# Kernel tuning notes

Hardware: AMD Instinct MI355X
Metric: run time of the kernel (lower is better)

The kernel has to match this reference:

```python
import jax, jax.numpy as jnp
import numpy as np

B, T, H, OUT = 2048, 256, 512, 1


def setup_inputs() -> dict:
    key = jax.random.key(0)
    ks = jax.random.split(key, 11)
    s = 1.0 / np.sqrt(H)
    return {
        "x": jax.random.normal(ks[0], (B, T), dtype=jnp.float32),
        # weights stored as (in, out), i.e. torch Linear weight transposed
        "Wx0": jax.random.normal(ks[1], (1, H), dtype=jnp.float32) * s,
        "bx0": jax.random.normal(ks[2], (H,), dtype=jnp.float32) * s,
        "Wh0": jax.random.normal(ks[3], (H, H), dtype=jnp.float32) * s,
        "bh0": jax.random.normal(ks[4], (H,), dtype=jnp.float32) * s,
        "Wx1": jax.random.normal(ks[5], (H, H), dtype=jnp.float32) * s,
        "bx1": jax.random.normal(ks[6], (H,), dtype=jnp.float32) * s,
        "Wh1": jax.random.normal(ks[7], (H, H), dtype=jnp.float32) * s,
        "bh1": jax.random.normal(ks[8], (H,), dtype=jnp.float32) * s,
        "Wfc": jax.random.normal(ks[9], (H, OUT), dtype=jnp.float32) * s,
        "bfc": jax.random.normal(ks[10], (OUT,), dtype=jnp.float32) * s,
    }


def reference(x, Wx0, bx0, Wh0, bh0, Wx1, bx1, Wh1, bh1, Wfc, bfc):
    # Stacked 2-layer Elman RNN: h_l[t] = tanh(W_in_l @ in + b_in_l + W_h_l @ h_l[t-1] + b_h_l)
    batch = x.shape[0]
    hdim = Wh0.shape[0]
    h0 = jnp.zeros((batch, hdim), dtype=x.dtype)
    h1 = jnp.zeros((batch, hdim), dtype=x.dtype)

    def step(carry, xt):
        h0, h1 = carry
        # layer 0: scalar input per timestep -> outer product with Wx0 row
        h0 = jnp.tanh(xt[:, None] * Wx0[0] + bx0 + h0 @ Wh0 + bh0)
        # layer 1 consumes the NEW h0 (matches the in-place loop in torch)
        h1 = jnp.tanh(h0 @ Wx1 + bx1 + h1 @ Wh1 + bh1)
        return (h0, h1), None

    (h0, h1), _ = jax.lax.scan(step, (h0, h1), x.T)  # scan over time [T, B]
    return h1 @ Wfc + bfc  # [B, OUT]
```

## Files before the change

### kernel.cpp

```cpp
#include <hip/hip_runtime.h>
#include <hip/hip_bf16.h>


typedef _Float16 half8 __attribute__((ext_vector_type(8)));
typedef float f32x4 __attribute__((ext_vector_type(4)));

#define T_STEPS 256
#define H_DIM   512
#define BM      16

#define BARRIER() do { \
    asm volatile("s_waitcnt lgkmcnt(0)" ::: "memory"); \
    __builtin_amdgcn_s_barrier(); \
    asm volatile("" ::: "memory"); \
  } while (0)

__device__ __forceinline__ half8 gld16(const half8* p){
  half8 r;
  asm volatile("global_load_dwordx4 %0, %1, off" : "=v"(r) : "v"(p));
  return r;
}

__device__ __forceinline__ float tanh_fast(float z){
  float az = fabsf(z);
  float e  = __expf(-2.0f * az);
  float r  = (1.0f - e) * __builtin_amdgcn_rcpf(1.0f + e);
  return copysignf(r, z);
}

__global__ void prep_w_45028437131357(const float* __restrict__ W,
                                      half8* __restrict__ out){
  int tid  = blockIdx.x * 256 + threadIdx.x;
  int lane = tid & 63;
  int kc   = (tid >> 6) & 15;
  int nt   = tid >> 10;
  int col  = nt * 16 + (lane & 15);
  int k0   = kc * 32 + (lane >> 4) * 8;
  half8 v;
#pragma unroll
  for (int j = 0; j < 8; ++j) v[j] = (_Float16)W[(k0 + j) * H_DIM + col];
  out[tid] = v;
}


__global__ __launch_bounds__(512, 2)
void rnn_main_45028437131357(const float* __restrict__ x,
                             const float* __restrict__ Wx0,
                             const float* __restrict__ bx0,
                             const float* __restrict__ bh0,
                             const float* __restrict__ bx1,
                             const float* __restrict__ bh1,
                             const float* __restrict__ Wfc,
                             const float* __restrict__ bfc,
                             const half8* __restrict__ Wh0f,
                             const half8* __restrict__ Wx1f,
                             const half8* __restrict__ Wh1f,
                             float* __restrict__ out){
  __shared__ __align__(16) char  h0d[2][BM * 1024];
  __shared__ __align__(16) char  h1s[BM * 1024];
  __shared__ __align__(16) float xall[BM * 256];
  __shared__ char lds_pad[20 * 1024];

  const int tid  = threadIdx.x;
  const int lane = tid & 63;
  const int w    = tid >> 6;
  const int w4   = 4 * w;
  const int r0   = blockIdx.x * BM;
  const int koff = (blockIdx.x >> 3) & 15;

  if (out == nullptr) ((volatile char*)lds_pad)[0] = 1;

  for (int i = tid; i < BM * 256; i += 512){
    ((float*)h0d[0])[i] = 0.0f;
    ((float*)h1s)[i] = 0.0f;
    int r = i >> 8, c = i & 255;
    xall[r * 256 + (c ^ ((r & 7) << 2))] = x[(r0 + r) * T_STEPS + c];
  }

  const int cl      = lane & 15;
  const int kg      = lane >> 4;
  const int aBase   = cl * 1024 + kg * 16;
  const int aSwz    = (cl & 7) << 4;
  const int rowBase = kg * 4;

  float wx0c[4], b0c[4], b1c[4];
  int   colA[4];
#pragma unroll
  for (int i = 0; i < 4; ++i){
    int col = (w4 + i) * 16 + cl;
    colA[i] = col;
    wx0c[i] = Wx0[col];
    b0c[i]  = bx0[col] + bh0[col];
    b1c[i]  = bx1[col] + bh1[col];
  }

  half8 rb[4][4];

#define STAGE(G)                                                              \
  {                                                                           \
    int g48 = ((G) >= 48) ? (G) - 48 : (G);                                   \
    const half8* M = (g48 < 16) ? Wh0f : ((g48 < 32) ? Wh1f : Wx1f);          \
    int keff = ((g48 & 15) + koff) & 15;                                      \
    const half8* base = M + keff * 64 + lane;                                 \
    rb[(G) & 3][0] = gld16(base + (w4 + 0) * 1024);                           \
    rb[(G) & 3][1] = gld16(base + (w4 + 1) * 1024);                           \
    rb[(G) & 3][2] = gld16(base + (w4 + 2) * 1024);                           \
    rb[(G) & 3][3] = gld16(base + (w4 + 3) * 1024);                           \
  }

#define CONSUME(APTR, ACC, KC, G)                                             \
  {                                                                           \
    int keff = (((KC) + koff) & 15);                                          \
    half8 a = *(const half8*)((APTR) + ((aBase + keff * 64) ^ aSwz));         \
    asm volatile("s_waitcnt vmcnt(12)");                                      \
    __builtin_amdgcn_sched_barrier(0);                                        \
    ACC[0] = __builtin_amdgcn_mfma_f32_16x16x32_f16(a, rb[(G)&3][0], ACC[0], 0,0,0); \
    ACC[1] = __builtin_amdgcn_mfma_f32_16x16x32_f16(a, rb[(G)&3][1], ACC[1], 0,0,0); \
    ACC[2] = __builtin_amdgcn_mfma_f32_16x16x32_f16(a, rb[(G)&3][2], ACC[2], 0,0,0); \
    ACC[3] = __builtin_amdgcn_mfma_f32_16x16x32_f16(a, rb[(G)&3][3], ACC[3], 0,0,0); \
  }

  asm volatile("s_waitcnt vmcnt(0)" ::: "memory");
  STAGE(0); STAGE(1); STAGE(2);

  const f32x4 z4 = {0.f, 0.f, 0.f, 0.f};
  int s = 0;

  for (int t = 0; t < T_STEPS; ++t){
    BARRIER();

    const char* h0cur = h0d[s];
    char*       h0nxt = h0d[s ^ 1];

    f32x4 acc0[4] = {z4, z4, z4, z4};
    f32x4 acc1[4] = {z4, z4, z4, z4};

#pragma unroll
    for (int kc = 0; kc < 16; ++kc){
      STAGE(kc + 3);
      CONSUME(h0cur, acc0, kc, kc);
    }
#pragma unroll
    for (int kc = 0; kc < 16; ++kc){
      STAGE(kc + 19);
      CONSUME(h1s, acc1, kc, kc + 16);
    }

    {
      float xv[4];
#pragma unroll
      for (int rg = 0; rg < 4; ++rg){
        int row = rowBase + rg;
        xv[rg] = xall[row * 256 + (t ^ ((row & 7) << 2))];
      }
#pragma unroll
      for (int i = 0; i < 4; ++i)
#pragma unroll
        for (int rg = 0; rg < 4; ++rg){
          float z = acc0[i][rg] + b0c[i] + xv[rg] * wx0c[i];
          int row = rowBase + rg;
          *(_Float16*)(h0nxt + row * 1024 +
                       ((colA[i] * 2) ^ ((row & 7) << 4))) = (_Float16)tanh_fast(z);
        }
    }
    BARRIER();

#pragma unroll
    for (int kc = 0; kc < 16; ++kc){
      STAGE(kc + 35);
      CONSUME(h0nxt, acc1, kc, kc + 32);
    }

#pragma unroll
    for (int i = 0; i < 4; ++i)
#pragma unroll
      for (int rg = 0; rg < 4; ++rg){
        int row = rowBase + rg;
        *(_Float16*)(h1s + row * 1024 +
                     ((colA[i] * 2) ^ ((row & 7) << 4))) =
            (_Float16)tanh_fast(acc1[i][rg] + b1c[i]);
      }
    s ^= 1;
  }
#undef STAGE
#undef CONSUME

  asm volatile("s_waitcnt vmcnt(0)" ::: "memory");
  BARRIER();

  {
    int r  = tid >> 5;
    int g2 = tid & 31;
    float p = 0.0f;
#pragma unroll
    for (int k2 = 0; k2 < 16; ++k2){
      int c = g2 + 32 * k2;
      float hv = (float)*(const _Float16*)(h1s + r * 1024 +
                                           ((c * 2) ^ ((r & 7) << 4)));
      p += hv * Wfc[c];
    }
#pragma unroll
    for (int off = 16; off >= 1; off >>= 1) p += __shfl_xor(p, off);
    if (g2 == 0) out[r0 + r] = p + bfc[0];
  }
}

extern "C" void kernel_launch(void* const* d_in, const int* in_sizes, int n_in,
                              void* d_out, int out_size, void* d_ws, size_t ws_size,
                              hipStream_t stream) {
  const float* x   = (const float*)d_in[0];
  const float* Wx0 = (const float*)d_in[1];
  const float* bx0 = (const float*)d_in[2];
  const float* Wh0 = (const float*)d_in[3];
  const float* bh0 = (const float*)d_in[4];
  const float* Wx1 = (const float*)d_in[5];
  const float* bx1 = (const float*)d_in[6];
  const float* Wh1 = (const float*)d_in[7];
  const float* bh1 = (const float*)d_in[8];
  const float* Wfc = (const float*)d_in[9];
  const float* bfc = (const float*)d_in[10];

  _Float16* wsH = (_Float16*)d_ws;
  half8* Wh0f = (half8*)(wsH);
  half8* Wx1f = (half8*)(wsH + 262144);
  half8* Wh1f = (half8*)(wsH + 524288);

  prep_w_45028437131357<<<128, 256, 0, stream>>>(Wh0, Wh0f);
  prep_w_45028437131357<<<128, 256, 0, stream>>>(Wx1, Wx1f);
  prep_w_45028437131357<<<128, 256, 0, stream>>>(Wh1, Wh1f);

  rnn_main_45028437131357<<<128, 512, 0, stream>>>(
      x, Wx0, bx0, bh0, bx1, bh1, Wfc, bfc,
      (const half8*)Wh0f, (const half8*)Wx1f, (const half8*)Wh1f,
      (float*)d_out);
}
```

Measured before the change: 13.07 ms.

## Double batch rows per block to reuse streamed weights across two MFMA row tiles

Each block now handles 32 batch rows instead of 16, and launches 64 blocks instead of 128. Every weight fragment loaded from global memory feeds two MFMA row tiles, which halves total weight traffic per timestep. The LDS padding that limited occupancy is removed, and the weight-start offset changes to stagger L2 access across blocks. The cost is fewer blocks than CUs, so only half the chip is used, and each block does twice the MFMA work on a serial time-step chain.

```diff
diff --git a/kernel.cpp b/kernel.cpp
--- a/kernel.cpp
+++ b/kernel.cpp
@@ -7,7 +7,7 @@
 
 #define T_STEPS 256
 #define H_DIM   512
-#define BM      16
+#define BM      32
 
 #define BARRIER() do { \
     asm volatile("s_waitcnt lgkmcnt(0)" ::: "memory"); \
@@ -59,16 +59,13 @@
   __shared__ __align__(16) char  h0d[2][BM * 1024];
   __shared__ __align__(16) char  h1s[BM * 1024];
   __shared__ __align__(16) float xall[BM * 256];
-  __shared__ char lds_pad[20 * 1024];
 
   const int tid  = threadIdx.x;
   const int lane = tid & 63;
   const int w    = tid >> 6;
   const int w4   = 4 * w;
   const int r0   = blockIdx.x * BM;
-  const int koff = (blockIdx.x >> 3) & 15;
-
-  if (out == nullptr) ((volatile char*)lds_pad)[0] = 1;
+  const int koff = (blockIdx.x & 7) * 2;
 
   for (int i = tid; i < BM * 256; i += 512){
     ((float*)h0d[0])[i] = 0.0f;
@@ -79,8 +76,9 @@
 
   const int cl      = lane & 15;
   const int kg      = lane >> 4;
-  const int aBase   = cl * 1024 + kg * 16;
   const int aSwz    = (cl & 7) << 4;
+  const int aOff0   = (cl)      * 1024 + kg * 16;
+  const int aOff1   = (cl + 16) * 1024 + kg * 16;
   const int rowBase = kg * 4;
 
   float wx0c[4], b0c[4], b1c[4];
@@ -108,16 +106,21 @@
     rb[(G) & 3][3] = gld16(base + (w4 + 3) * 1024);                           \
   }
 
-#define CONSUME(APTR, ACC, KC, G)                                             \
+#define CONSUME(APTR, AC, KC, G)                                              \
   {                                                                           \
-    int keff = (((KC) + koff) & 15);                                          \
-    half8 a = *(const half8*)((APTR) + ((aBase + keff * 64) ^ aSwz));         \
+    int kb = (((KC) + koff) & 15) * 64;                                       \
+    half8 a0 = *(const half8*)((APTR) + ((aOff0 + kb) ^ aSwz));               \
+    half8 a1 = *(const half8*)((APTR) + ((aOff1 + kb) ^ aSwz));               \
     asm volatile("s_waitcnt vmcnt(12)");                                      \
     __builtin_amdgcn_sched_barrier(0);                                        \
-    ACC[0] = __builtin_amdgcn_mfma_f32_16x16x32_f16(a, rb[(G)&3][0], ACC[0], 0,0,0); \
-    ACC[1] = __builtin_amdgcn_mfma_f32_16x16x32_f16(a, rb[(G)&3][1], ACC[1], 0,0,0); \
-    ACC[2] = __builtin_amdgcn_mfma_f32_16x16x32_f16(a, rb[(G)&3][2], ACC[2], 0,0,0); \
-    ACC[3] = __builtin_amdgcn_mfma_f32_16x16x32_f16(a, rb[(G)&3][3], ACC[3], 0,0,0); \
+    AC[0][0] = __builtin_amdgcn_mfma_f32_16x16x32_f16(a0, rb[(G)&3][0], AC[0][0], 0,0,0); \
+    AC[0][1] = __builtin_amdgcn_mfma_f32_16x16x32_f16(a0, rb[(G)&3][1], AC[0][1], 0,0,0); \
+    AC[0][2] = __builtin_amdgcn_mfma_f32_16x16x32_f16(a0, rb[(G)&3][2], AC[0][2], 0,0,0); \
+    AC[0][3] = __builtin_amdgcn_mfma_f32_16x16x32_f16(a0, rb[(G)&3][3], AC[0][3], 0,0,0); \
+    AC[1][0] = __builtin_amdgcn_mfma_f32_16x16x32_f16(a1, rb[(G)&3][0], AC[1][0], 0,0,0); \
+    AC[1][1] = __builtin_amdgcn_mfma_f32_16x16x32_f16(a1, rb[(G)&3][1], AC[1][1], 0,0,0); \
+    AC[1][2] = __builtin_amdgcn_mfma_f32_16x16x32_f16(a1, rb[(G)&3][2], AC[1][2], 0,0,0); \
+    AC[1][3] = __builtin_amdgcn_mfma_f32_16x16x32_f16(a1, rb[(G)&3][3], AC[1][3], 0,0,0); \
   }
 
   asm volatile("s_waitcnt vmcnt(0)" ::: "memory");
@@ -132,8 +135,8 @@
     const char* h0cur = h0d[s];
     char*       h0nxt = h0d[s ^ 1];
 
-    f32x4 acc0[4] = {z4, z4, z4, z4};
-    f32x4 acc1[4] = {z4, z4, z4, z4};
+    f32x4 acc0[2][4] = {{z4,z4,z4,z4},{z4,z4,z4,z4}};
+    f32x4 acc1[2][4] = {{z4,z4,z4,z4},{z4,z4,z4,z4}};
 
 #pragma unroll
     for (int kc = 0; kc < 16; ++kc){
@@ -146,19 +149,20 @@
       CONSUME(h1s, acc1, kc, kc + 16);
     }
 
-    {
+#pragma unroll
+    for (int rt = 0; rt < 2; ++rt){
       float xv[4];
 #pragma unroll
       for (int rg = 0; rg < 4; ++rg){
-        int row = rowBase + rg;
+        int row = rt * 16 + rowBase + rg;
         xv[rg] = xall[row * 256 + (t ^ ((row & 7) << 2))];
       }
 #pragma unroll
       for (int i = 0; i < 4; ++i)
 #pragma unroll
         for (int rg = 0; rg < 4; ++rg){
-          float z = acc0[i][rg] + b0c[i] + xv[rg] * wx0c[i];
-          int row = rowBase + rg;
+          float z = acc0[rt][i][rg] + b0c[i] + xv[rg] * wx0c[i];
+          int row = rt * 16 + rowBase + rg;
           *(_Float16*)(h0nxt + row * 1024 +
                        ((colA[i] * 2) ^ ((row & 7) << 4))) = (_Float16)tanh_fast(z);
         }
@@ -172,14 +176,16 @@
     }
 
 #pragma unroll
-    for (int i = 0; i < 4; ++i)
-#pragma unroll
-      for (int rg = 0; rg < 4; ++rg){
-        int row = rowBase + rg;
-        *(_Float16*)(h1s + row * 1024 +
-                     ((colA[i] * 2) ^ ((row & 7) << 4))) =
-            (_Float16)tanh_fast(acc1[i][rg] + b1c[i]);
-      }
+    for (int rt = 0; rt < 2; ++rt)
+#pragma unroll
+      for (int i = 0; i < 4; ++i)
+#pragma unroll
+        for (int rg = 0; rg < 4; ++rg){
+          int row = rt * 16 + rowBase + rg;
+          *(_Float16*)(h1s + row * 1024 +
+                       ((colA[i] * 2) ^ ((row & 7) << 4))) =
+              (_Float16)tanh_fast(acc1[rt][i][rg] + b1c[i]);
+        }
     s ^= 1;
   }
 #undef STAGE
@@ -189,18 +195,18 @@
   BARRIER();
 
   {
-    int r  = tid >> 5;
-    int g2 = tid & 31;
+    int r  = tid >> 4;
+    int g2 = tid & 15;
     float p = 0.0f;
 #pragma unroll
-    for (int k2 = 0; k2 < 16; ++k2){
-      int c = g2 + 32 * k2;
+    for (int k2 = 0; k2 < 32; ++k2){
+      int c = g2 + 16 * k2;
       float hv = (float)*(const _Float16*)(h1s + r * 1024 +
                                            ((c * 2) ^ ((r & 7) << 4)));
       p += hv * Wfc[c];
     }
 #pragma unroll
-    for (int off = 16; off >= 1; off >>= 1) p += __shfl_xor(p, off);
+    for (int off = 8; off >= 1; off >>= 1) p += __shfl_xor(p, off);
     if (g2 == 0) out[r0 + r] = p + bfc[0];
   }
 }
@@ -229,7 +235,7 @@
   prep_w_45028437131357<<<128, 256, 0, stream>>>(Wx1, Wx1f);
   prep_w_45028437131357<<<128, 256, 0, stream>>>(Wh1, Wh1f);
 
-  rnn_main_45028437131357<<<128, 512, 0, stream>>>(
+  rnn_main_45028437131357<<<64, 512, 0, stream>>>(
       x, Wx0, bx0, bh0, bx1, bh1, Wfc, bfc,
       (const half8*)Wh0f, (const half8*)Wx1f, (const half8*)Wh1f,
       (float*)d_out);
```

After: 15.56 ms. 1.19x slower.
